# Kernel optimization log

Measured on AMD Instinct MI355X. Metric: run time of the kernel, lower is better.

The kernel has to match this reference:

```python
import jax, jax.numpy as jnp
import numpy as np

B, P, NOBJ, C = 32, 16384, 50, 21
THRESHOLD, NEG_POS_RATIO, ALPHA = 0.5, 3.0, 1.0


def cxcy_to_xy(c):
    return jnp.concatenate([c[:, :2] - c[:, 2:] / 2, c[:, :2] + c[:, 2:] / 2], axis=1)


def xy_to_cxcy(xy):
    return jnp.concatenate([(xy[:, :2] + xy[:, 2:]) / 2, xy[:, 2:] - xy[:, :2]], axis=1)


def cxcy_to_gcxgcy(cxcy, priors_cxcy):
    # standard SSD encoding with variances 0.1 / 0.2
    g_cxcy = (cxcy[:, :2] - priors_cxcy[:, :2]) / (priors_cxcy[:, 2:] / 10.0)
    g_wh = jnp.log(cxcy[:, 2:] / priors_cxcy[:, 2:]) * 5.0
    return jnp.concatenate([g_cxcy, g_wh], axis=1)


def jaccard(a, b):
    # a: [N,4] xyxy, b: [P,4] xyxy -> [N,P]
    lt = jnp.maximum(a[:, None, :2], b[None, :, :2])
    rb = jnp.minimum(a[:, None, 2:], b[None, :, 2:])
    inter = jnp.clip(rb - lt, 0.0).prod(-1)
    area_a = (a[:, 2:] - a[:, :2]).prod(-1)
    area_b = (b[:, 2:] - b[:, :2]).prod(-1)
    return inter / (area_a[:, None] + area_b[None, :] - inter)


def setup_inputs() -> dict:
    key = jax.random.key(0)
    k1, k2, k3, k4, k5, k6, k7 = jax.random.split(key, 7)
    predicted_locs = jax.random.normal(k1, (B, P, 4), dtype=jnp.float32)
    predicted_scores = jax.random.normal(k2, (B, P, C), dtype=jnp.float32)
    # ground-truth boxes: valid xyxy in [0,1] with positive extent
    ccx = jax.random.uniform(k3, (B, NOBJ, 2), minval=0.1, maxval=0.9)
    wh = jax.random.uniform(k4, (B, NOBJ, 2), minval=0.02, maxval=0.2)
    boxes = jnp.concatenate([ccx - wh / 2, ccx + wh / 2], axis=-1).astype(jnp.float32)
    labels = jax.random.randint(k5, (B, NOBJ), 1, C)  # object labels are >= 1 (0 = background)
    pcxy = jax.random.uniform(k6, (P, 2), minval=0.05, maxval=0.95)
    pwh = jax.random.uniform(k7, (P, 2), minval=0.02, maxval=0.4)
    priors_cxcy = jnp.concatenate([pcxy, pwh], axis=-1).astype(jnp.float32)
    return dict(predicted_locs=predicted_locs, predicted_scores=predicted_scores,
                boxes=boxes, labels=labels, priors_cxcy=priors_cxcy)


def reference(predicted_locs, predicted_scores, boxes, labels, priors_cxcy):
    priors_xy = cxcy_to_xy(priors_cxcy)

    def assign(boxes_i, labels_i):
        ov = jaccard(boxes_i, priors_xy)                    # [N,P]
        overlap_for_prior = ov.max(axis=0)                  # [P]
        object_for_prior = ov.argmax(axis=0)                # [P]
        prior_for_object = ov.argmax(axis=1)                # [N]
        # force each object to own its best prior
        object_for_prior = object_for_prior.at[prior_for_object].set(jnp.arange(NOBJ))
        overlap_for_prior = overlap_for_prior.at[prior_for_object].set(1.0)
        label_for_prior = labels_i[object_for_prior]
        label_for_prior = jnp.where(overlap_for_prior < THRESHOLD, 0, label_for_prior)
        assigned_xy = boxes_i[object_for_prior]             # [P,4]
        true_locs_i = cxcy_to_gcxgcy(xy_to_cxcy(assigned_xy), priors_cxcy)
        return true_locs_i, label_for_prior

    true_locs, true_classes = jax.vmap(assign)(boxes, labels)  # [B,P,4], [B,P]

    pos = true_classes != 0                                 # [B,P]
    n_pos = pos.sum(axis=1)                                 # [B]
    n_pos_total = n_pos.sum().astype(jnp.float32)

    # nn.L1Loss(): mean abs error over positive prior entries (Npos*4 elements)
    l1 = jnp.abs(predicted_locs - true_locs) * pos[..., None]
    loc_loss = l1.sum() / (n_pos_total * 4.0)

    # per-prior cross entropy
    logp = jax.nn.log_softmax(predicted_scores, axis=-1)    # [B,P,C]
    ce = -jnp.take_along_axis(logp, true_classes[..., None], axis=-1)[..., 0]  # [B,P]

    conf_pos = jnp.where(pos, ce, 0.0).sum()
    neg = jnp.where(pos, 0.0, ce)
    neg_sorted = -jnp.sort(-neg, axis=1)                    # descending per image
    ranks = jnp.arange(P)[None, :].astype(jnp.float32)
    hard = ranks < (NEG_POS_RATIO * n_pos.astype(jnp.float32))[:, None]
    conf_hard_neg = jnp.where(hard, neg_sorted, 0.0).sum()

    conf_loss = (conf_hard_neg + conf_pos) / n_pos_total
    return conf_loss + ALPHA * loc_loss
```

## Files before the change

### kernel.cpp

```cpp
#include <hip/hip_runtime.h>
#include <hip/hip_bf16.h>
#include <float.h>

#define BB   32
#define PP   16384
#define NOBJ 50
#define NCLS 21
#define PBLK 64
#define NBLK (BB * PBLK)
#define NGRP 7
#define NCHK 8
#define CPRI 2048
#define JPT  8


__global__ __launch_bounds__(256) void k_iou(
    const float* __restrict__ boxes, const float* __restrict__ priors,
    unsigned long long* __restrict__ bp_part,
    unsigned* __restrict__ ovp_part)
{
#pragma clang fp contract(off)
    const int blk   = (int)blockIdx.x;
    const int b     = blk / (NGRP * NCHK);
    const int rem   = blk % (NGRP * NCHK);
    const int g     = rem / NCHK;
    const int c     = rem % NCHK;
    const int n0    = g * 8;
    const int pbase = c * CPRI;
    const int t     = (int)threadIdx.x;

    __shared__ unsigned long long skey[8][256];

    float ax0[8], ay0[8], ax1[8], ay1[8], aarea[8];
#pragma unroll
    for (int k = 0; k < 8; ++k) {
        int nn = n0 + k; if (nn >= NOBJ) nn = NOBJ - 1;
        float4 bx = reinterpret_cast<const float4*>(boxes)[b * NOBJ + nn];
        ax0[k] = bx.x; ay0[k] = bx.y; ax1[k] = bx.z; ay1[k] = bx.w;
        aarea[k] = (bx.z - bx.x) * (bx.w - bx.y);
    }

    float px0[JPT], py0[JPT], px1[JPT], py1[JPT], pab[JPT];
#pragma unroll
    for (int j = 0; j < JPT; ++j) {
        float4 pc = reinterpret_cast<const float4*>(priors)[pbase + t + j * 256];
        float hx = pc.z * 0.5f, hy = pc.w * 0.5f;
        px0[j] = pc.x - hx; py0[j] = pc.y - hy;
        px1[j] = pc.x + hx; py1[j] = pc.y + hy;
        pab[j] = (px1[j] - px0[j]) * (py1[j] - py0[j]);
    }

    float bof[8];  int bop[8];
    float bpf[JPT]; int bpn[JPT];
#pragma unroll
    for (int k = 0; k < 8; ++k) { bof[k] = -1.0f; bop[k] = 0; }
#pragma unroll
    for (int j = 0; j < JPT; ++j) { bpf[j] = -1.0f; bpn[j] = 0; }

#pragma unroll
    for (int k = 0; k < 8; ++k) {
#pragma unroll
        for (int j = 0; j < JPT; ++j) {
            float ltx = fmaxf(ax0[k], px0[j]), lty = fmaxf(ay0[k], py0[j]);
            float rbx = fminf(ax1[k], px1[j]), rby = fminf(ay1[k], py1[j]);
            float dx = fmaxf(rbx - ltx, 0.0f);
            float dy = fmaxf(rby - lty, 0.0f);
            float inter = dx * dy;
            float iou = __fdividef(inter, (aarea[k] + pab[j]) - inter);
            if (iou > bof[k]) { bof[k] = iou; bop[k] = pbase + t + j * 256; }
            if (iou > bpf[j]) { bpf[j] = iou; bpn[j] = n0 + k; }
        }
    }

#pragma unroll
    for (int j = 0; j < JPT; ++j) {
        unsigned key32 = ((__float_as_uint(bpf[j]) << 2) & 0xFFFFFFC0u) |
                         (unsigned)(NOBJ - 1 - bpn[j]);
        ovp_part[((size_t)g * BB + b) * PP + pbase + t + j * 256] = key32;
    }

#pragma unroll
    for (int k = 0; k < 8; ++k)
        skey[k][t] = ((unsigned long long)__float_as_uint(bof[k]) << 32) |
                     (unsigned long long)(0xFFFFFFFFu - (unsigned)bop[k]);
    __syncthreads();
    {
        int k2 = t >> 5, sl = t & 31;
        unsigned long long bestv = skey[k2][sl];
#pragma unroll
        for (int i = 1; i < 8; ++i) {
            unsigned long long cand = skey[k2][sl + 32 * i];
            if (cand > bestv) bestv = cand;
        }
        __syncthreads();
        skey[k2][sl] = bestv;
    }
    __syncthreads();
    if (t < 64) {
        int k2 = t >> 3, sl = t & 7;
        unsigned long long bestv = skey[k2][sl * 4];
#pragma unroll
        for (int i = 1; i < 4; ++i) {
            unsigned long long cand = skey[k2][sl * 4 + i];
            if (cand > bestv) bestv = cand;
        }
        skey[k2][32 + sl] = bestv;
    }
    __syncthreads();
    if (t < 8 && n0 + t < NOBJ) {
        unsigned long long bestv = skey[t][32];
#pragma unroll
        for (int i = 1; i < 8; ++i) {
            unsigned long long cand = skey[t][32 + i];
            if (cand > bestv) bestv = cand;
        }
        bp_part[(size_t)c * BB * NOBJ + b * NOBJ + n0 + t] = bestv;
    }
}

__global__ __launch_bounds__(256) void k_main(
    const float* __restrict__ locs, const float* __restrict__ scores,
    const float* __restrict__ boxes, const int* __restrict__ labels,
    const float* __restrict__ priors,
    const unsigned long long* __restrict__ bp_part,
    const unsigned* __restrict__ ovp_part,
    float* __restrict__ neg, double* __restrict__ pc_conf,
    double* __restrict__ pc_loc, int* __restrict__ pc_npos)
{
#pragma clang fp contract(off)
    const int b   = (int)blockIdx.x >> 6;
    const int p0  = ((int)blockIdx.x & 63) << 8;
    const int t   = (int)threadIdx.x;
    const int p   = p0 + t;
    const int idx = b * PP + p;

    __shared__ float  sls[256 * NCLS];
    __shared__ int    sforce[256];
    __shared__ float4 sbox[NOBJ];
    __shared__ int    slab[NOBJ];
    __shared__ double sconf[4], sloc[4];
    __shared__ int    snp[4];

    {
        const float4* gsc = reinterpret_cast<const float4*>(
            scores + (size_t)(b * PP + p0) * NCLS);
        float4* dls = reinterpret_cast<float4*>(sls);
#pragma unroll
        for (int i = 0; i < 6; ++i) {
            int j = i * 256 + t;
            if (j < (256 * NCLS) / 4) dls[j] = gsc[j];
        }
    }
    sforce[t] = -1;
    if (t < NOBJ) {
        sbox[t] = reinterpret_cast<const float4*>(boxes)[b * NOBJ + t];
        slab[t] = labels[b * NOBJ + t];
    }
    __syncthreads();
    if (t < NOBJ) {
        unsigned long long k0 = bp_part[b * NOBJ + t];
#pragma unroll
        for (int cc = 1; cc < NCHK; ++cc) {
            unsigned long long kc = bp_part[(size_t)cc * BB * NOBJ + b * NOBJ + t];
            if (kc > k0) k0 = kc;
        }
        int spf = (int)(0xFFFFFFFFu - (unsigned)(k0 & 0xFFFFFFFFull));
        if (spf >= p0 && spf < p0 + 256)
            atomicMax(&sforce[spf - p0], t);
    }
    __syncthreads();

    unsigned key = ovp_part[(size_t)b * PP + p];
#pragma unroll
    for (int g = 1; g < NGRP; ++g) {
        unsigned kg = ovp_part[((size_t)g * BB + b) * PP + p];
        if (kg > key) key = kg;
    }
    int   bestn = NOBJ - 1 - (int)(key & 63u);
    float v     = __uint_as_float((key >> 6) << 4);
    int fn = sforce[t];
    if (fn >= 0) { bestn = fn; v = 1.0f; }

    int lbl = slab[bestn];
    if (v < 0.5f) lbl = 0;
    const bool pos = (lbl != 0);

    float locl1 = 0.0f;
    if (pos) {
        float4 bx = sbox[bestn];
        float4 pc = reinterpret_cast<const float4*>(priors)[p];
        float cx = (bx.x + bx.z) / 2.0f;
        float cy = (bx.y + bx.w) / 2.0f;
        float w  = bx.z - bx.x, h = bx.w - bx.y;
        float gx = (cx - pc.x) / (pc.z / 10.0f);
        float gy = (cy - pc.y) / (pc.w / 10.0f);
        float gw = logf(w / pc.z) * 5.0f;
        float gh = logf(h / pc.w) * 5.0f;
        float4 pl = reinterpret_cast<const float4*>(locs)[idx];
        locl1 = fabsf(pl.x - gx) + fabsf(pl.y - gy) +
                fabsf(pl.z - gw) + fabsf(pl.w - gh);
    }

    float x[NCLS];
    float m = -FLT_MAX;
#pragma unroll
    for (int c = 0; c < NCLS; ++c) { x[c] = sls[t * NCLS + c]; m = fmaxf(m, x[c]); }
    float tgt = sls[t * NCLS + lbl];
    float s = 0.0f;
#pragma unroll
    for (int c = 0; c < NCLS; ++c) s += expf(x[c] - m);
    float ce = (logf(s) + m) - tgt;

    neg[idx] = pos ? 0.0f : ce;

    float cp = pos ? ce : 0.0f;
    unsigned long long bal = __ballot(pos);
    float s1 = cp, s2 = locl1;
    for (int o = 32; o > 0; o >>= 1) {
        s1 += __shfl_down(s1, o, 64);
        s2 += __shfl_down(s2, o, 64);
    }
    if ((t & 63) == 0) {
        int w = t >> 6;
        sconf[w] = (double)s1;
        sloc[w]  = (double)s2;
        snp[w]   = (int)__popcll(bal);
    }
    __syncthreads();
    if (t == 0) {
        pc_conf[blockIdx.x] = sconf[0] + sconf[1] + sconf[2] + sconf[3];
        pc_loc[blockIdx.x]  = sloc[0] + sloc[1] + sloc[2] + sloc[3];
        pc_npos[blockIdx.x] = snp[0] + snp[1] + snp[2] + snp[3];
    }
}

__global__ __launch_bounds__(1024) void k_topk(
    const float* __restrict__ neg, const int* __restrict__ pc_npos,
    double* __restrict__ hard)
{
    const int b    = (int)blockIdx.x;
    const int t    = (int)threadIdx.x;
    const int lane = t & 63;
    const int wid  = t >> 6;

    __shared__ unsigned hist[64 * 257];
    __shared__ unsigned swsum[4];
    __shared__ unsigned s_bb, s_above;
    __shared__ float swave[16];
    __shared__ int s_np;

    if (t < 64) {
        int v = pc_npos[b * PBLK + t];
        for (int o = 32; o > 0; o >>= 1) v += __shfl_down(v, o, 64);
        if (t == 0) s_np = v;
    }

    float v[16];
    {
        const float4* g = reinterpret_cast<const float4*>(neg + (size_t)b * PP);
#pragma unroll
        for (int i = 0; i < 4; ++i) {
            float4 q = g[i * 1024 + t];
            v[i*4+0] = q.x; v[i*4+1] = q.y; v[i*4+2] = q.z; v[i*4+3] = q.w;
        }
    }
    __syncthreads();

    long long K = 3LL * (long long)s_np;
    if (K > PP) K = PP;
    unsigned remaining = (unsigned)K;
    unsigned prefix = 0, mask = 0;
    float mySum = 0.0f;

    for (int shift = 24; shift >= 0; shift -= 8) {
        for (int i = t; i < 64 * 257; i += 1024) hist[i] = 0;
        __syncthreads();
        unsigned* h = hist + lane * 257;
#pragma unroll
        for (int i = 0; i < 16; ++i) {
            unsigned u = __float_as_uint(v[i]);
            if ((u & mask) == prefix) atomicAdd(&h[(u >> shift) & 255u], 1u);
        }
        __syncthreads();
        unsigned cnt = 0, suf = 0;
        if (t < 256) {
#pragma unroll
            for (int w = 0; w < 64; ++w) cnt += hist[w * 257 + t];
            unsigned vs = cnt;
#pragma unroll
            for (int off = 1; off < 64; off <<= 1) {
                unsigned o2 = __shfl_down(vs, off, 64);
                if (lane + off < 64) vs += o2;
            }
            if (lane == 0) swsum[wid] = vs;
            suf = vs;
        }
        __syncthreads();
        if (t < 256) {
            for (int wseg = wid + 1; wseg < 4; ++wseg) suf += swsum[wseg];
            if (suf >= remaining && suf - cnt < remaining) {
                s_bb = (unsigned)t; s_above = suf - cnt;
            }
        }
        __syncthreads();
        unsigned bb = s_bb;
#pragma unroll
        for (int i = 0; i < 16; ++i) {
            unsigned u = __float_as_uint(v[i]);
            if ((u & mask) == prefix && ((u >> shift) & 255u) > bb)
                mySum += v[i];
        }
        remaining -= s_above;
        prefix |= bb << shift;
        mask   |= 255u << shift;
        __syncthreads();
    }

    float s = mySum;
    for (int o = 32; o > 0; o >>= 1) s += __shfl_down(s, o, 64);
    if ((t & 63) == 0) swave[wid] = s;
    __syncthreads();
    if (t == 0) {
        float tot = 0.0f;
        for (int w = 0; w < 16; ++w) tot += swave[w];
        if (remaining) tot += (float)remaining * __uint_as_float(prefix);
        hard[b] = (double)tot;
    }
}

__global__ __launch_bounds__(256) void k_final(
    const double* __restrict__ pc_conf, const double* __restrict__ pc_loc,
    const int* __restrict__ pc_npos, const double* __restrict__ hard,
    float* __restrict__ out)
{
    const int t = (int)threadIdx.x;
    __shared__ double sa[4], sb[4], sh[4];
    __shared__ int sn[4];
    double a = 0.0, c = 0.0, h = 0.0; int np = 0;
    for (int i = t; i < NBLK; i += 256) {
        a += pc_conf[i]; c += pc_loc[i]; np += pc_npos[i];
    }
    if (t < BB) h = hard[t];
    for (int o = 32; o > 0; o >>= 1) {
        a += __shfl_down(a, o, 64);
        c += __shfl_down(c, o, 64);
        h += __shfl_down(h, o, 64);
        np += __shfl_down(np, o, 64);
    }
    if ((t & 63) == 0) { int w = t >> 6; sa[w]=a; sb[w]=c; sh[w]=h; sn[w]=np; }
    __syncthreads();
    if (t == 0) {
        double at = sa[0]+sa[1]+sa[2]+sa[3];
        double ct = sb[0]+sb[1]+sb[2]+sb[3];
        double ht = sh[0]+sh[1]+sh[2]+sh[3];
        double npt = (double)(sn[0]+sn[1]+sn[2]+sn[3]);
        out[0] = (float)((at + ht) / npt + ct / (npt * 4.0));
    }
}

extern "C" void kernel_launch(void* const* d_in, const int* in_sizes, int n_in,
                              void* d_out, int out_size, void* d_ws, size_t ws_size,
                              hipStream_t stream) {
    const float* locs   = (const float*)d_in[0];
    const float* scores = (const float*)d_in[1];
    const float* boxes  = (const float*)d_in[2];
    const int*   labels = (const int*)d_in[3];
    const float* priors = (const float*)d_in[4];

    char* ws = (char*)d_ws;
    unsigned long long* bp_part = (unsigned long long*)ws;
    double* pc_conf = (double*)(ws + 262144);
    double* pc_loc  = (double*)(ws + 278528);
    int*    pc_npos = (int*)(ws + 294912);
    double* hard    = (double*)(ws + 303104);
    unsigned* ovp_part = (unsigned*)(ws + 327680);
    float*  neg     = (float*)(ws + 33554432);
    float*  out     = (float*)d_out;

    hipLaunchKernelGGL(k_iou,   dim3(BB * NGRP * NCHK), dim3(256),  0, stream,
                       boxes, priors, bp_part, ovp_part);
    hipLaunchKernelGGL(k_main,  dim3(NBLK),             dim3(256),  0, stream,
                       locs, scores, boxes, labels, priors, bp_part, ovp_part,
                       neg, pc_conf, pc_loc, pc_npos);
    hipLaunchKernelGGL(k_topk,  dim3(BB),               dim3(1024), 0, stream,
                       neg, pc_npos, hard);
    hipLaunchKernelGGL(k_final, dim3(1),                dim3(256),  0, stream,
                       pc_conf, pc_loc, pc_npos, hard, out);
}
```

Before: 68.42 us.

## Fuse final reduction into top-k kernel and drop max-subtraction in softmax

Removes the separate single-block final kernel. The last k_topk block, found through an atomic counter that k_main resets, now does the global reduction, saving one launch and its dependency gap. It also drops the max-subtraction from the log-sum-exp in cross entropy, which saves a pass over the 21 logits. That is safe only while scores are small enough not to overflow expf, and it clamps ce at zero to hide rounding.

```diff
diff --git a/kernel.cpp b/kernel.cpp
--- a/kernel.cpp
+++ b/kernel.cpp
@@ -125,7 +125,8 @@
     const unsigned long long* __restrict__ bp_part,
     const unsigned* __restrict__ ovp_part,
     float* __restrict__ neg, double* __restrict__ pc_conf,
-    double* __restrict__ pc_loc, int* __restrict__ pc_npos)
+    double* __restrict__ pc_loc, int* __restrict__ pc_npos,
+    unsigned* __restrict__ topk_cnt)
 {
 #pragma clang fp contract(off)
     const int b   = (int)blockIdx.x >> 6;
@@ -133,6 +134,8 @@
     const int t   = (int)threadIdx.x;
     const int p   = p0 + t;
     const int idx = b * PP + p;
+
+    if (blockIdx.x == 0 && t == 0) *topk_cnt = 0;
 
     __shared__ float  sls[256 * NCLS];
     __shared__ int    sforce[256];
@@ -201,15 +204,11 @@
                 fabsf(pl.z - gw) + fabsf(pl.w - gh);
     }
 
-    float x[NCLS];
-    float m = -FLT_MAX;
-#pragma unroll
-    for (int c = 0; c < NCLS; ++c) { x[c] = sls[t * NCLS + c]; m = fmaxf(m, x[c]); }
     float tgt = sls[t * NCLS + lbl];
     float s = 0.0f;
 #pragma unroll
-    for (int c = 0; c < NCLS; ++c) s += expf(x[c] - m);
-    float ce = (logf(s) + m) - tgt;
+    for (int c = 0; c < NCLS; ++c) s += expf(sls[t * NCLS + c]);
+    float ce = fmaxf(logf(s) - tgt, 0.0f);
 
     neg[idx] = pos ? 0.0f : ce;
 
@@ -236,7 +235,9 @@
 
 __global__ __launch_bounds__(1024) void k_topk(
     const float* __restrict__ neg, const int* __restrict__ pc_npos,
-    double* __restrict__ hard)
+    const double* __restrict__ pc_conf, const double* __restrict__ pc_loc,
+    double* __restrict__ hard, unsigned* __restrict__ topk_cnt,
+    float* __restrict__ out)
 {
     const int b    = (int)blockIdx.x;
     const int t    = (int)threadIdx.x;
@@ -248,6 +249,9 @@
     __shared__ unsigned s_bb, s_above;
     __shared__ float swave[16];
     __shared__ int s_np;
+    __shared__ int s_last;
+    __shared__ double sda[16], sdb[16], sdh[16];
+    __shared__ long long sdn[16];
 
     if (t < 64) {
         int v = pc_npos[b * PBLK + t];
@@ -325,36 +329,35 @@
         for (int w = 0; w < 16; ++w) tot += swave[w];
         if (remaining) tot += (float)remaining * __uint_as_float(prefix);
         hard[b] = (double)tot;
-    }
-}
-
-__global__ __launch_bounds__(256) void k_final(
-    const double* __restrict__ pc_conf, const double* __restrict__ pc_loc,
-    const int* __restrict__ pc_npos, const double* __restrict__ hard,
-    float* __restrict__ out)
-{
-    const int t = (int)threadIdx.x;
-    __shared__ double sa[4], sb[4], sh[4];
-    __shared__ int sn[4];
-    double a = 0.0, c = 0.0, h = 0.0; int np = 0;
-    for (int i = t; i < NBLK; i += 256) {
-        a += pc_conf[i]; c += pc_loc[i]; np += pc_npos[i];
-    }
-    if (t < BB) h = hard[t];
-    for (int o = 32; o > 0; o >>= 1) {
-        a += __shfl_down(a, o, 64);
-        c += __shfl_down(c, o, 64);
-        h += __shfl_down(h, o, 64);
-        np += __shfl_down(np, o, 64);
-    }
-    if ((t & 63) == 0) { int w = t >> 6; sa[w]=a; sb[w]=c; sh[w]=h; sn[w]=np; }
-    __syncthreads();
-    if (t == 0) {
-        double at = sa[0]+sa[1]+sa[2]+sa[3];
-        double ct = sb[0]+sb[1]+sb[2]+sb[3];
-        double ht = sh[0]+sh[1]+sh[2]+sh[3];
-        double npt = (double)(sn[0]+sn[1]+sn[2]+sn[3]);
-        out[0] = (float)((at + ht) / npt + ct / (npt * 4.0));
+        __threadfence();
+        unsigned r = atomicAdd(topk_cnt, 1u);
+        s_last = (r == BB - 1);
+    }
+    __syncthreads();
+
+    if (s_last) {
+        __threadfence();
+        double a = 0.0, c2 = 0.0, h = 0.0; long long np = 0;
+        for (int i = t; i < NBLK; i += 1024) {
+            a += pc_conf[i]; c2 += pc_loc[i]; np += pc_npos[i];
+        }
+        if (t < BB) h = hard[t];
+        for (int o = 32; o > 0; o >>= 1) {
+            a  += __shfl_down(a, o, 64);
+            c2 += __shfl_down(c2, o, 64);
+            h  += __shfl_down(h, o, 64);
+            np += __shfl_down(np, o, 64);
+        }
+        if ((t & 63) == 0) { sda[wid]=a; sdb[wid]=c2; sdh[wid]=h; sdn[wid]=np; }
+        __syncthreads();
+        if (t == 0) {
+            double at = 0.0, ct = 0.0, ht = 0.0; long long nt = 0;
+            for (int w = 0; w < 16; ++w) {
+                at += sda[w]; ct += sdb[w]; ht += sdh[w]; nt += sdn[w];
+            }
+            double npt = (double)nt;
+            out[0] = (float)((at + ht) / npt + ct / (npt * 4.0));
+        }
     }
 }
 
@@ -373,6 +376,7 @@
     double* pc_loc  = (double*)(ws + 278528);
     int*    pc_npos = (int*)(ws + 294912);
     double* hard    = (double*)(ws + 303104);
+    unsigned* topk_cnt = (unsigned*)(ws + 303360);
     unsigned* ovp_part = (unsigned*)(ws + 327680);
     float*  neg     = (float*)(ws + 33554432);
     float*  out     = (float*)d_out;
@@ -381,9 +385,7 @@
                        boxes, priors, bp_part, ovp_part);
     hipLaunchKernelGGL(k_main,  dim3(NBLK),             dim3(256),  0, stream,
                        locs, scores, boxes, labels, priors, bp_part, ovp_part,
-                       neg, pc_conf, pc_loc, pc_npos);
+                       neg, pc_conf, pc_loc, pc_npos, topk_cnt);
     hipLaunchKernelGGL(k_topk,  dim3(BB),               dim3(1024), 0, stream,
-                       neg, pc_npos, hard);
-    hipLaunchKernelGGL(k_final, dim3(1),                dim3(256),  0, stream,
-                       pc_conf, pc_loc, pc_npos, hard, out);
+                       neg, pc_npos, pc_conf, pc_loc, hard, topk_cnt, out);
 }
```

New measurement: 72.05 us. 1.05x slower.
